# Kernel optimization log

Hardware: AMD Instinct MI355X
Metric: run time of the kernel (lower is better)

The kernel has to match this reference:

```python
import jax, jax.numpy as jnp
import numpy as np

B = 128      # graphs per side
N = 512      # nodes per graph (max for dense batch)
TOT = B * N  # 65536 total nodes per side
FIN = 128
F1, F2, F3 = 64, 64, 32
TN = 16      # tensor_neurons
BINS = 16
BN = 16      # bottleneck neurons
E = 16 * TOT # edges per side


def setup_inputs() -> dict:
    key = jax.random.key(0)
    ks = jax.random.split(key, 20)
    nrm = lambda k, shape, s=0.1: (jax.random.normal(k, shape, jnp.float32) * s)
    batch = jnp.repeat(jnp.arange(B, dtype=jnp.int32), N)
    return {
        'x1': jax.random.normal(ks[0], (TOT, FIN), jnp.float32),
        'x2': jax.random.normal(ks[1], (TOT, FIN), jnp.float32),
        'edge_index_1': jax.random.randint(ks[2], (2, E), 0, TOT, jnp.int32),
        'edge_index_2': jax.random.randint(ks[3], (2, E), 0, TOT, jnp.int32),
        'batch_1': batch,
        'batch_2': batch,
        'W1': nrm(ks[4], (FIN, F1)), 'b1': jnp.zeros((F1,), jnp.float32),
        'W2': nrm(ks[5], (F1, F2)), 'b2': jnp.zeros((F2,), jnp.float32),
        'W3': nrm(ks[6], (F2, F3)), 'b3': jnp.zeros((F3,), jnp.float32),
        'att_W': nrm(ks[7], (F3, F3)),
        'ntn_W': nrm(ks[8], (F3, F3, TN)),
        'ntn_V': nrm(ks[9], (TN, 2 * F3)),
        'ntn_b': jnp.zeros((TN,), jnp.float32),
        'fc1_W': nrm(ks[10], (TN + BINS, BN)),
        'fc1_b': jnp.zeros((BN,), jnp.float32),
        'sc_W': nrm(ks[11], (BN, 1)),
        'sc_b': jnp.zeros((1,), jnp.float32),
    }


def _gcn(x, W, b, src, dst):
    # PyG GCNConv: h = XW; add self-loops; D^{-1/2} A D^{-1/2} aggregation; + bias
    h = x @ W
    deg = jnp.zeros((TOT,), jnp.float32).at[dst].add(1.0) + 1.0  # incl. self-loop
    dis = jax.lax.rsqrt(deg)
    msg = h[src] * (dis[src] * dis[dst])[:, None]
    out = jnp.zeros_like(h).at[dst].add(msg) + h * (1.0 / deg)[:, None]
    return out + b


def _conv_pass(x, ei, W1, b1, W2, b2, W3, b3):
    # dropout is identity in eval mode
    h = jax.nn.relu(_gcn(x, W1, b1, ei[0], ei[1]))
    h = jax.nn.relu(_gcn(h, W2, b2, ei[0], ei[1]))
    return _gcn(h, W3, b3, ei[0], ei[1])


def _to_dense_batch(x, batch):
    ones = jnp.ones((TOT,), jnp.float32)
    cnt = jax.ops.segment_sum(ones, batch, num_segments=B)  # [B]
    starts = jnp.concatenate([jnp.zeros((1,), jnp.int32), jnp.cumsum(cnt.astype(jnp.int32))[:-1]])
    pos = jnp.arange(TOT, dtype=jnp.int32) - starts[batch]
    dense = jnp.zeros((B, N, x.shape[1]), x.dtype).at[batch, pos].set(x)
    cnt_i = cnt.astype(jnp.int32)
    return dense, cnt_i


def _histogram(af1, af2, batch_1, batch_2):
    d1, cnt1 = _to_dense_batch(af1, batch_1)
    d2, cnt2 = _to_dense_batch(af2, batch_2)
    nn = jnp.maximum(cnt1, cnt2)  # [B]
    sc = jax.nn.sigmoid(jax.lax.stop_gradient(jnp.einsum('bnf,bmf->bnm', d1, d2)))  # [B,N,N]
    ar = jnp.arange(N)
    valid = (ar[None, :, None] < nn[:, None, None]) & (ar[None, None, :] < nn[:, None, None])
    big = jnp.float32(1e30)
    mn = jnp.min(jnp.where(valid, sc, big), axis=(1, 2))
    mx = jnp.max(jnp.where(valid, sc, -big), axis=(1, 2))
    rng = jnp.where(mx > mn, mx - mn, jnp.float32(1.0))
    bidx = jnp.clip(jnp.floor((sc - mn[:, None, None]) / rng[:, None, None] * BINS), 0, BINS - 1).astype(jnp.int32)
    ids = jnp.arange(B, dtype=jnp.int32)[:, None, None] * BINS + bidx
    hist = jnp.zeros((B * BINS,), jnp.float32).at[ids.reshape(-1)].add(valid.reshape(-1).astype(jnp.float32))
    hist = hist.reshape(B, BINS)
    return hist / hist.sum(axis=1, keepdims=True)


def _att_pool(h, batch, att_W):
    cnt = jax.ops.segment_sum(jnp.ones((TOT,), jnp.float32), batch, num_segments=B)
    g = jax.ops.segment_sum(h @ att_W, batch, num_segments=B) / cnt[:, None]
    t = jnp.tanh(g)                                   # [B,F3] global context
    s = jax.nn.sigmoid(jnp.sum(h * t[batch], axis=1)) # [TOT] attention
    return jax.ops.segment_sum(h * s[:, None], batch, num_segments=B)


def reference(x1, x2, edge_index_1, edge_index_2, batch_1, batch_2,
              W1, b1, W2, b2, W3, b3, att_W, ntn_W, ntn_V, ntn_b,
              fc1_W, fc1_b, sc_W, sc_b):
    af1 = _conv_pass(x1, edge_index_1, W1, b1, W2, b2, W3, b3)
    af2 = _conv_pass(x2, edge_index_2, W1, b1, W2, b2, W3, b3)
    hist = _histogram(af1, af2, batch_1, batch_2)
    p1 = _att_pool(af1, batch_1, att_W)
    p2 = _att_pool(af2, batch_2, att_W)
    # Neural Tensor Network
    bilin = jnp.einsum('bi,ijk,bj->bk', p1, ntn_W, p2)
    blk = jnp.concatenate([p1, p2], axis=1) @ ntn_V.T
    scores = jax.nn.relu(bilin + blk + ntn_b)
    feat = jnp.concatenate([scores, hist], axis=1)
    h = jax.nn.relu(feat @ fc1_W + fc1_b)
    return jax.nn.sigmoid(h @ sc_W + sc_b).reshape(-1)
```

## Files before the change

kernel.cpp:

```cpp
#include <hip/hip_runtime.h>
#include <hip/hip_bf16.h>

constexpr int    TOT = 65536;
constexpr int    TOT2 = 131072;
constexpr long long Ec = 16LL * TOT;
constexpr int    NB  = 1024;
constexpr int    BKN = 128;
constexpr int    CAP = 2816;

typedef unsigned int   uint32;
typedef unsigned short ushort16;
typedef __attribute__((ext_vector_type(8))) short bf16x8;
typedef __attribute__((ext_vector_type(4))) float f32x4;

__device__ __forceinline__ float sigm(float x) { return 1.f / (1.f + __expf(-x)); }

__device__ __forceinline__ uint32 f2bf_rne(float x) {
    uint32 u = __float_as_uint(x);
    return (u + 0x7fffu + ((u >> 16) & 1u)) >> 16;
}
__device__ __forceinline__ float2 bf2f(uint32 u) {
    return make_float2(__uint_as_float(u << 16), __uint_as_float(u & 0xffff0000u));
}
__device__ __forceinline__ float bf1f(ushort16 u) {
    return __uint_as_float(((uint32)u) << 16);
}
__device__ __forceinline__ uint32 relu_bf2(uint32 v) {
    uint32 keep = (((int)v < 0) ? 0u : 0xFFFF0000u) | ((v & 0x8000u) ? 0u : 0x0000FFFFu);
    return v & keep;
}

__global__ void setup_k(const float* __restrict__ W1, const float* __restrict__ W2,
                        const float* __restrict__ W3, ushort16* __restrict__ Wt1,
                        ushort16* __restrict__ Wt2, ushort16* __restrict__ Wt3,
                        const int* __restrict__ b1, const int* __restrict__ b2,
                        int* __restrict__ cnt, int* __restrict__ st,
                        int* __restrict__ gcnt, float* __restrict__ hist) {
    int t = blockIdx.x * 256 + threadIdx.x;
    if (t < 8192) {
        int j = t >> 7, k = t & 127;
        Wt1[t] = (ushort16)f2bf_rne(W1[k * 64 + j]);
    } else if (t < 12288) {
        int u = t - 8192; int j = u >> 6, k = u & 63;
        Wt2[u] = (ushort16)f2bf_rne(W2[k * 64 + j]);
    } else if (t < 14336) {
        int u = t - 12288; int j = u >> 6, k = u & 63;
        Wt3[u] = (ushort16)f2bf_rne(W3[k * 32 + j]);
    } else if (t < 14592) {
        int q = t - 14336;
        const int* bat = (q < 128) ? b1 : b2;
        const int g = q & 127;
        int lo = 0, hi = TOT;
        while (lo < hi) { int m = (lo + hi) >> 1; if (bat[m] < g) lo = m + 1; else hi = m; }
        const int s0 = lo;
        hi = TOT;
        while (lo < hi) { int m = (lo + hi) >> 1; if (bat[m] < g + 1) lo = m + 1; else hi = m; }
        st[q] = s0;
        cnt[q] = lo - s0;
    } else if (t < 15616) {
        gcnt[t - 14592] = 0;
    } else if (t < 17664) {
        hist[t - 15616] = 0.f;
    }
}

__global__ __launch_bounds__(1024) void bktfill2_k(const int* __restrict__ ei1, const int* __restrict__ ei2,
                                                   int* __restrict__ gcnt, uint32* __restrict__ bkt) {
    __shared__ int hist[NB];
    __shared__ int hbase[NB];
    const int tid = threadIdx.x, blk = blockIdx.x;
    hist[tid] = 0;
    __syncthreads();
    const long long base = (long long)blk * 8192;
#pragma unroll
    for (int q = 0; q < 8; ++q) {
        long long e = base + q * 1024 + tid;
        int d = (e < Ec) ? ei1[Ec + e] : (TOT + ei2[Ec + (e - Ec)]);
        atomicAdd(&hist[d >> 7], 1);
    }
    __syncthreads();
    {
        int c = hist[tid];
        hbase[tid] = c ? atomicAdd(&gcnt[tid], c) : 0;
        hist[tid] = 0;
    }
    __syncthreads();
#pragma unroll
    for (int q = 0; q < 8; ++q) {
        long long e = base + q * 1024 + tid;
        int s, d;
        if (e < Ec) { s = ei1[e]; d = ei1[Ec + e]; }
        else        { long long e2 = e - Ec; s = TOT + ei2[e2]; d = TOT + ei2[Ec + e2]; }
        int bb = d >> 7;
        int lofs = atomicAdd(&hist[bb], 1);
        bkt[(size_t)bb * CAP + hbase[bb] + lofs] = (uint32)s | ((uint32)(d & 127) << 20);
    }
}

__global__ __launch_bounds__(256) void bktsort_k(const int* __restrict__ gcnt, const uint32* __restrict__ bkt,
                                                 uint32* __restrict__ csr, int* __restrict__ rowstart,
                                                 int* __restrict__ rowend, float* __restrict__ dis) {
    __shared__ int deg[BKN], offs[BKN], cur[BKN];
    const int b = blockIdx.x, tid = threadIdx.x;
    const int ne = gcnt[b];
    const int e0 = b * CAP;
    if (tid < BKN) deg[tid] = 0;
    __syncthreads();
    for (int i = tid; i < ne; i += 256) atomicAdd(&deg[bkt[e0 + i] >> 20], 1);
    __syncthreads();
    if (tid == 0) {
        int o = 0;
        for (int q = 0; q < BKN; ++q) { offs[q] = o; cur[q] = o; o += deg[q]; }
    }
    __syncthreads();
    if (tid < BKN) {
        rowstart[b * BKN + tid] = e0 + offs[tid];
        rowend[b * BKN + tid]   = e0 + offs[tid] + deg[tid];
        dis[b * BKN + tid] = rsqrtf((float)deg[tid] + 1.0f);
    }
    __syncthreads();
    for (int i = tid; i < ne; i += 256) {
        uint32 v = bkt[e0 + i];
        int dl = v >> 20;
        int pos = atomicAdd(&cur[dl], 1);
        csr[e0 + pos] = v & 0x1FFFF;
    }
}

template<int K, int NC, bool RELU, bool XBF>
__global__ __launch_bounds__(256) void gemmf_k(const void* __restrict__ X1v,
                                               const void* __restrict__ X2v,
                                               const ushort16* __restrict__ Wt,
                                               const float* __restrict__ dis,
                                               ushort16* __restrict__ out) {
    constexpr int NK = K / 32;
    const int tid = threadIdx.x, lane = tid & 63, wave = tid >> 6;
    const int i0 = (blockIdx.x * 4 + wave) * 16;
    const int arow = i0 + (lane & 15);
    const int ks0 = (lane >> 4) * 8;
    bf16x8 a[NK];
    if (XBF) {
        const uint32* Xr = (arow < TOT) ? (const uint32*)X1v + (size_t)arow * (K / 2)
                                        : (const uint32*)X2v + (size_t)(arow - TOT) * (K / 2);
#pragma unroll
        for (int s = 0; s < NK; ++s) {
            uint4 v = *(const uint4*)(Xr + s * 16 + ks0 / 2);
            if (RELU) { v.x = relu_bf2(v.x); v.y = relu_bf2(v.y); v.z = relu_bf2(v.z); v.w = relu_bf2(v.w); }
            a[s] = *(bf16x8*)&v;
        }
    } else {
        const float* Xr = (arow < TOT) ? (const float*)X1v + (size_t)arow * K
                                       : (const float*)X2v + (size_t)(arow - TOT) * K;
#pragma unroll
        for (int s = 0; s < NK; ++s) {
            float4 v0 = *(const float4*)(Xr + s * 32 + ks0);
            float4 v1 = *(const float4*)(Xr + s * 32 + ks0 + 4);
            if (RELU) {
                v0.x = fmaxf(v0.x, 0.f); v0.y = fmaxf(v0.y, 0.f); v0.z = fmaxf(v0.z, 0.f); v0.w = fmaxf(v0.w, 0.f);
                v1.x = fmaxf(v1.x, 0.f); v1.y = fmaxf(v1.y, 0.f); v1.z = fmaxf(v1.z, 0.f); v1.w = fmaxf(v1.w, 0.f);
            }
            uint4 p;
            p.x = f2bf_rne(v0.x) | (f2bf_rne(v0.y) << 16);
            p.y = f2bf_rne(v0.z) | (f2bf_rne(v0.w) << 16);
            p.z = f2bf_rne(v1.x) | (f2bf_rne(v1.y) << 16);
            p.w = f2bf_rne(v1.z) | (f2bf_rne(v1.w) << 16);
            a[s] = *(bf16x8*)&p;
        }
    }
    float dv[4];
#pragma unroll
    for (int r = 0; r < 4; ++r) dv[r] = dis[i0 + (lane >> 4) * 4 + r];
#pragma unroll
    for (int jt = 0; jt < NC / 16; ++jt) {
        const int col = jt * 16 + (lane & 15);
        f32x4 cc = {0.f, 0.f, 0.f, 0.f};
#pragma unroll
        for (int s = 0; s < NK; ++s) {
            bf16x8 b = *(const bf16x8*)(Wt + (size_t)col * K + s * 32 + ks0);
            cc = __builtin_amdgcn_mfma_f32_16x16x32_bf16(a[s], b, cc, 0, 0, 0);
        }
#pragma unroll
        for (int r = 0; r < 4; ++r) {
            const int row = i0 + (lane >> 4) * 4 + r;
            out[(size_t)row * NC + col] = (ushort16)f2bf_rne(cc[r] * dv[r]);
        }
    }
}

template<int NC>
__global__ __launch_bounds__(256) void gatherb_k(uint32* __restrict__ out, const uint32* __restrict__ hs,
                                                 const float* __restrict__ dis, const float* __restrict__ bias,
                                                 const int* __restrict__ rowstart, const int* __restrict__ rowend,
                                                 const uint32* __restrict__ csr) {
    constexpr int TPN = NC / 2;
    constexpr int NG  = 256 / TPN;
    constexpr int NPB = 2 * NG;
    int bid;
    {
        const int xcd = blockIdx.x & 7, idx = blockIdx.x >> 3;
        const int half = gridDim.x >> 1;
        bid = (xcd < 4) ? (idx * 4 + xcd) : (half + idx * 4 + (xcd - 4));
    }
    const int tid = threadIdx.x;
    const int cp = tid & (TPN - 1);
    const int g = tid / TPN;
    const int nodeA = bid * NPB + g;
    const int nodeB = nodeA + NG;
    const float2 bb = ((const float2*)bias)[cp];
    float2 svA = bf2f(hs[(size_t)nodeA * TPN + cp]);
    float2 svB = bf2f(hs[(size_t)nodeB * TPN + cp]);
    float a0 = svA.x, a1 = svA.y;
    float b0 = svB.x, b1 = svB.y;
    int eA = rowstart[nodeA]; const int eA1 = rowend[nodeA];
    int eB = rowstart[nodeB]; const int eB1 = rowend[nodeB];
    while (true) {
        const bool ca = (eA + 8 <= eA1), cb = (eB + 8 <= eB1);
        if (!ca && !cb) break;
        uint32 pa[8], pb[8];
        if (ca) {
#pragma unroll
            for (int q = 0; q < 8; ++q) pa[q] = hs[(size_t)csr[eA + q] * TPN + cp];
        }
        if (cb) {
#pragma unroll
            for (int q = 0; q < 8; ++q) pb[q] = hs[(size_t)csr[eB + q] * TPN + cp];
        }
        if (ca) {
#pragma unroll
            for (int q = 0; q < 8; ++q) { float2 f = bf2f(pa[q]); a0 += f.x; a1 += f.y; }
            eA += 8;
        }
        if (cb) {
#pragma unroll
            for (int q = 0; q < 8; ++q) { float2 f = bf2f(pb[q]); b0 += f.x; b1 += f.y; }
            eB += 8;
        }
    }
    if (eA + 4 <= eA1) {
        uint32 p[4];
#pragma unroll
        for (int q = 0; q < 4; ++q) p[q] = hs[(size_t)csr[eA + q] * TPN + cp];
#pragma unroll
        for (int q = 0; q < 4; ++q) { float2 f = bf2f(p[q]); a0 += f.x; a1 += f.y; }
        eA += 4;
    }
    for (; eA < eA1; ++eA) { float2 f = bf2f(hs[(size_t)csr[eA] * TPN + cp]); a0 += f.x; a1 += f.y; }
    if (eB + 4 <= eB1) {
        uint32 p[4];
#pragma unroll
        for (int q = 0; q < 4; ++q) p[q] = hs[(size_t)csr[eB + q] * TPN + cp];
#pragma unroll
        for (int q = 0; q < 4; ++q) { float2 f = bf2f(p[q]); b0 += f.x; b1 += f.y; }
        eB += 4;
    }
    for (; eB < eB1; ++eB) { float2 f = bf2f(hs[(size_t)csr[eB] * TPN + cp]); b0 += f.x; b1 += f.y; }
    const float dvA = dis[nodeA], dvB = dis[nodeB];
    out[(size_t)nodeA * TPN + cp] = f2bf_rne(a0 * dvA + bb.x) | (f2bf_rne(a1 * dvA + bb.y) << 16);
    out[(size_t)nodeB * TPN + cp] = f2bf_rne(b0 * dvB + bb.x) | (f2bf_rne(b1 * dvB + bb.y) << 16);
}

__global__ __launch_bounds__(256) void attpool_k(const ushort16* __restrict__ af,
                                                 const int* __restrict__ cnt, const int* __restrict__ st,
                                                 const float* __restrict__ attW, float* __restrict__ pool) {
    const int side = blockIdx.x >> 7, b = blockIdx.x & 127;
    const ushort16* h = af + (size_t)side * TOT * 32;
    const int c = cnt[side * 128 + b], s0 = st[side * 128 + b];
    const int f = threadIdx.x & 31, grp = threadIdx.x >> 5;
    __shared__ float red[8][32];
    __shared__ float mhS[32], tS[32];
    float acc = 0.f;
    for (int i = grp; i < c; i += 8) acc += bf1f(h[(size_t)(s0 + i) * 32 + f]);
    red[grp][f] = acc;
    __syncthreads();
    if (threadIdx.x < 32) { float tt = 0; for (int g = 0; g < 8; ++g) tt += red[g][f]; mhS[f] = tt / (float)c; }
    __syncthreads();
    if (threadIdx.x < 32) {
        float g = 0;
        for (int k = 0; k < 32; ++k) g += mhS[k] * attW[k * 32 + f];
        tS[f] = tanhf(g);
    }
    __syncthreads();
    const float tf = tS[f];
    acc = 0.f;
    for (int i = grp; i < c; i += 8) {
        float hv = bf1f(h[(size_t)(s0 + i) * 32 + f]);
        float pr = hv * tf;
#pragma unroll
        for (int m = 16; m; m >>= 1) pr += __shfl_xor(pr, m, 32);
        float sA = 1.f / (1.f + expf(-pr));
        acc += hv * sA;
    }
    __syncthreads();
    red[grp][f] = acc;
    __syncthreads();
    if (threadIdx.x < 32) {
        float tt = 0; for (int g = 0; g < 8; ++g) tt += red[g][f];
        pool[(size_t)(side * 128 + b) * 32 + f] = tt;
    }
}

__global__ __launch_bounds__(256) void mm2_k(const ushort16* __restrict__ afb,
                                             const int* __restrict__ cnt, const int* __restrict__ st,
                                             float* __restrict__ bmn, float* __restrict__ bmx) {
    const int b = blockIdx.x >> 3, it8 = blockIdx.x & 7;
    const int c1 = cnt[b], c2 = cnt[128 + b];
    const int s1 = st[b], s2 = st[128 + b];
    const int nn = max(c1, c2);
    const int tid = threadIdx.x, lane = tid & 63, wave = tid >> 6;
    const int itile = it8 * 4 + wave;
    const int i0 = itile * 16;
    float lmn = 1e30f, lmx = -1e30f;
    if (i0 < nn) {
        const int arow = i0 + (lane & 15);
        const int koff = (lane >> 4) * 8;
        bf16x8 a = {0, 0, 0, 0, 0, 0, 0, 0};
        if (arow < c1) a = *(const bf16x8*)(afb + (size_t)(s1 + arow) * 32 + koff);
        const int ibase = i0 + (lane >> 4) * 4;
        const int njt = (nn + 15) >> 4;
        for (int jt = 0; jt < njt; ++jt) {
            const int brow = jt * 16 + (lane & 15);
            bf16x8 bb = {0, 0, 0, 0, 0, 0, 0, 0};
            if (brow < c2) bb = *(const bf16x8*)(afb + (size_t)(s2 + brow) * 32 + koff);
            f32x4 cc = {0.f, 0.f, 0.f, 0.f};
            cc = __builtin_amdgcn_mfma_f32_16x16x32_bf16(a, bb, cc, 0, 0, 0);
            if (brow < nn) {
#pragma unroll
                for (int r = 0; r < 4; ++r) {
                    if (ibase + r < nn) { lmn = fminf(lmn, cc[r]); lmx = fmaxf(lmx, cc[r]); }
                }
            }
        }
    }
    __shared__ float redn[256], redx[256];
    redn[tid] = lmn; redx[tid] = lmx;
    __syncthreads();
    for (int sr = 128; sr; sr >>= 1) {
        if (tid < sr) {
            redn[tid] = fminf(redn[tid], redn[tid + sr]);
            redx[tid] = fmaxf(redx[tid], redx[tid + sr]);
        }
        __syncthreads();
    }
    if (tid == 0) { bmn[blockIdx.x] = redn[0]; bmx[blockIdx.x] = redx[0]; }
}

__global__ __launch_bounds__(256) void bin2_k(const ushort16* __restrict__ afb,
                                              const int* __restrict__ cnt, const int* __restrict__ st,
                                              const float* __restrict__ bmn, const float* __restrict__ bmx,
                                              float* __restrict__ hist) {
    const int b = blockIdx.x >> 3, it8 = blockIdx.x & 7;
    const int c1 = cnt[b], c2 = cnt[128 + b];
    const int s1 = st[b], s2 = st[128 + b];
    const int nn = max(c1, c2);
    const int tid = threadIdx.x, lane = tid & 63, wave = tid >> 6;
    const int itile = it8 * 4 + wave;
    const int i0 = itile * 16;
    float dmn = 1e30f, dmx = -1e30f;
#pragma unroll
    for (int q = 0; q < 8; ++q) {
        dmn = fminf(dmn, bmn[(b << 3) + q]);
        dmx = fmaxf(dmx, bmx[(b << 3) + q]);
    }
    const float vMn = sigm(dmn), vMx = sigm(dmx);
    const float vScale = 16.f / ((vMx > vMn) ? (vMx - vMn) : 1.f);
    __shared__ int hloc[16 * 256];
    __shared__ int part[64];
#pragma unroll
    for (int q = 0; q < 16; ++q) hloc[q * 256 + tid] = 0;
    __syncthreads();
    if (i0 < nn) {
        const int arow = i0 + (lane & 15);
        const int koff = (lane >> 4) * 8;
        bf16x8 a = {0, 0, 0, 0, 0, 0, 0, 0};
        if (arow < c1) a = *(const bf16x8*)(afb + (size_t)(s1 + arow) * 32 + koff);
        const int ibase = i0 + (lane >> 4) * 4;
        const int njt = (nn + 15) >> 4;
        for (int jt = 0; jt < njt; ++jt) {
            const int brow = jt * 16 + (lane & 15);
            bf16x8 bb = {0, 0, 0, 0, 0, 0, 0, 0};
            if (brow < c2) bb = *(const bf16x8*)(afb + (size_t)(s2 + brow) * 32 + koff);
            f32x4 cc = {0.f, 0.f, 0.f, 0.f};
            cc = __builtin_amdgcn_mfma_f32_16x16x32_bf16(a, bb, cc, 0, 0, 0);
            if (brow < nn) {
#pragma unroll
                for (int r = 0; r < 4; ++r) {
                    if (ibase + r < nn) {
                        float t = (sigm(cc[r]) - vMn) * vScale;
                        int bi = (int)floorf(t);
                        bi = bi < 0 ? 0 : (bi > 15 ? 15 : bi);
                        hloc[bi * 256 + tid] += 1;
                    }
                }
            }
        }
    }
    __syncthreads();
    if (tid < 64) {
        const int bin = tid & 15, q = tid >> 4;
        int s = 0;
        for (int t2 = q * 64; t2 < q * 64 + 64; ++t2) s += hloc[bin * 256 + t2];
        part[tid] = s;
    }
    __syncthreads();
    if (tid < 16) {
        int s = part[tid] + part[16 + tid] + part[32 + tid] + part[48 + tid];
        atomicAdd(&hist[b * 16 + tid], (float)s);
    }
}

__global__ __launch_bounds__(64) void final_k(const float* __restrict__ pool, const float* __restrict__ hist,
                                              const int* __restrict__ cnt,
                                              const float* __restrict__ ntnW, const float* __restrict__ ntnV,
                                              const float* __restrict__ ntnb, const float* __restrict__ fc1W,
                                              const float* __restrict__ fc1b, const float* __restrict__ scW,
                                              const float* __restrict__ scb, float* __restrict__ out) {
    const int b = blockIdx.x;
    const int tid = threadIdx.x;
    __shared__ float P1[32], P2[32], feat[32], red[64];
    if (tid < 32) { P1[tid] = pool[b * 32 + tid]; P2[tid] = pool[4096 + b * 32 + tid]; }
    __syncthreads();
    const int k = tid & 15, part = tid >> 4;
    float acc = 0.f;
    for (int i = part * 8; i < part * 8 + 8; ++i) {
        float p1i = P1[i];
        for (int j = 0; j < 32; ++j) acc += p1i * P2[j] * ntnW[(i * 32 + j) * 16 + k];
    }
    red[tid] = acc;
    __syncthreads();
    if (tid < 16) {
        float bl = red[tid] + red[16 + tid] + red[32 + tid] + red[48 + tid];
        float blk = ntnb[tid];
        for (int i = 0; i < 32; ++i) blk += P1[i] * ntnV[tid * 64 + i];
        for (int j = 0; j < 32; ++j) blk += P2[j] * ntnV[tid * 64 + 32 + j];
        feat[tid] = fmaxf(bl + blk, 0.f);
        const int nn = max(cnt[b], cnt[128 + b]);
        feat[16 + tid] = hist[b * 16 + tid] / (float)(nn * nn);
    }
    __syncthreads();
    if (tid < 16) {
        float h = fc1b[tid];
        for (int f = 0; f < 32; ++f) h += feat[f] * fc1W[f * 16 + tid];
        red[tid] = fmaxf(h, 0.f);
    }
    __syncthreads();
    if (tid == 0) {
        float o = scb[0];
        for (int j = 0; j < 16; ++j) o += red[j] * scW[j];
        out[b] = 1.f / (1.f + expf(-o));
    }
}

extern "C" void kernel_launch(void* const* d_in, const int* in_sizes, int n_in,
                              void* d_out, int out_size, void* d_ws, size_t ws_size,
                              hipStream_t stream) {
    const float* x1   = (const float*)d_in[0];
    const float* x2   = (const float*)d_in[1];
    const int*   ei1  = (const int*)d_in[2];
    const int*   ei2  = (const int*)d_in[3];
    const int*   bat1 = (const int*)d_in[4];
    const int*   bat2 = (const int*)d_in[5];
    const float* W1   = (const float*)d_in[6];
    const float* b1   = (const float*)d_in[7];
    const float* W2   = (const float*)d_in[8];
    const float* b2   = (const float*)d_in[9];
    const float* W3   = (const float*)d_in[10];
    const float* b3   = (const float*)d_in[11];
    const float* attW = (const float*)d_in[12];
    const float* ntnW = (const float*)d_in[13];
    const float* ntnV = (const float*)d_in[14];
    const float* ntnb = (const float*)d_in[15];
    const float* fc1W = (const float*)d_in[16];
    const float* fc1b = (const float*)d_in[17];
    const float* scW  = (const float*)d_in[18];
    const float* scb  = (const float*)d_in[19];
    float* out = (float*)d_out;

    uint32* Hbuf   = (uint32*)d_ws;
    uint32* Gb     = Hbuf + (size_t)TOT2 * 32;
    uint32* AFb    = Gb + (size_t)TOT2 * 32;
    uint32* bkt    = AFb + (size_t)TOT2 * 16;
    uint32* csr    = bkt + (size_t)NB * CAP;
    float* dis     = (float*)(csr + (size_t)NB * CAP);
    int*   rowstart= (int*)(dis + TOT2);
    int*   rowend  = rowstart + TOT2;
    int*   gcnt    = rowend + TOT2;
    int*   cnt     = gcnt + NB;
    int*   st      = cnt + 256;
    float* pool    = (float*)(st + 256);
    float* hist    = pool + 8192;
    float* bmn     = hist + 2048;
    float* bmx     = bmn + 1024;
    ushort16* Wt1  = (ushort16*)(bmx + 1024);
    ushort16* Wt2  = Wt1 + 8192;
    ushort16* Wt3  = Wt2 + 4096;

    setup_k<<<69, 256, 0, stream>>>(W1, W2, W3, Wt1, Wt2, Wt3, bat1, bat2, cnt, st, gcnt, hist);
    bktfill2_k<<<256, 1024, 0, stream>>>(ei1, ei2, gcnt, bkt);
    bktsort_k<<<NB, 256, 0, stream>>>(gcnt, bkt, csr, rowstart, rowend, dis);

    gemmf_k<128, 64, false, false><<<2048, 256, 0, stream>>>(x1, x2, Wt1, dis, (ushort16*)Hbuf);
    gatherb_k<64><<<TOT2 / 16, 256, 0, stream>>>(Gb, Hbuf, dis, b1, rowstart, rowend, csr);

    gemmf_k<64, 64, true, true><<<2048, 256, 0, stream>>>(Gb, Gb, Wt2, dis, (ushort16*)Hbuf);
    gatherb_k<64><<<TOT2 / 16, 256, 0, stream>>>(Gb, Hbuf, dis, b2, rowstart, rowend, csr);

    gemmf_k<64, 32, true, true><<<2048, 256, 0, stream>>>(Gb, Gb, Wt3, dis, (ushort16*)Hbuf);
    gatherb_k<32><<<TOT2 / 32, 256, 0, stream>>>(AFb, Hbuf, dis, b3, rowstart, rowend, csr);

    attpool_k<<<256, 256, 0, stream>>>((const ushort16*)AFb, cnt, st, attW, pool);
    mm2_k<<<1024, 256, 0, stream>>>((const ushort16*)AFb, cnt, st, bmn, bmx);
    bin2_k<<<1024, 256, 0, stream>>>((const ushort16*)AFb, cnt, st, bmn, bmx, hist);
    final_k<<<128, 64, 0, stream>>>(pool, hist, cnt, ntnW, ntnV, ntnb, fc1W, fc1b, scW, scb, out);
}
```

Before: 315.3 us.

## Fuse GCN neighbor aggregation with next layer's MFMA GEMM

Adds an agemm_k kernel that gathers each node's CSR neighbors, applies the self-loop term, degree scaling, bias and ReLU in registers, then feeds the result directly into the next layer's bf16 MFMA projection. This replaces two gather+GEMM kernel pairs, removing the intermediate bf16 write and reread and two launches. In exchange, each MFMA lane now performs a 16-row gather with 8-wide unrolled neighbor loads. That can raise register pressure and gives less parallel gather work than the dedicated gather kernel.

Result: faster. 298.8 us (-5.2%).

```diff
diff --git a/kernel.cpp b/kernel.cpp
--- a/kernel.cpp
+++ b/kernel.cpp
@@ -28,6 +28,11 @@
 __device__ __forceinline__ uint32 relu_bf2(uint32 v) {
     uint32 keep = (((int)v < 0) ? 0u : 0xFFFF0000u) | ((v & 0x8000u) ? 0u : 0x0000FFFFu);
     return v & keep;
+}
+__device__ __forceinline__ void addu4(float* a, uint4 v) {
+    float2 f0 = bf2f(v.x), f1 = bf2f(v.y), f2 = bf2f(v.z), f3 = bf2f(v.w);
+    a[0] += f0.x; a[1] += f0.y; a[2] += f1.x; a[3] += f1.y;
+    a[4] += f2.x; a[5] += f2.y; a[6] += f3.x; a[7] += f3.y;
 }
 
 __global__ void setup_k(const float* __restrict__ W1, const float* __restrict__ W2,
@@ -127,9 +132,9 @@
     }
 }
 
-template<int K, int NC, bool RELU, bool XBF>
-__global__ __launch_bounds__(256) void gemmf_k(const void* __restrict__ X1v,
-                                               const void* __restrict__ X2v,
+template<int K, int NC>
+__global__ __launch_bounds__(256) void gemmf_k(const float* __restrict__ X1,
+                                               const float* __restrict__ X2,
                                                const ushort16* __restrict__ Wt,
                                                const float* __restrict__ dis,
                                                ushort16* __restrict__ out) {
@@ -139,26 +144,13 @@
     const int arow = i0 + (lane & 15);
     const int ks0 = (lane >> 4) * 8;
     bf16x8 a[NK];
-    if (XBF) {
-        const uint32* Xr = (arow < TOT) ? (const uint32*)X1v + (size_t)arow * (K / 2)
-                                        : (const uint32*)X2v + (size_t)(arow - TOT) * (K / 2);
-#pragma unroll
-        for (int s = 0; s < NK; ++s) {
-            uint4 v = *(const uint4*)(Xr + s * 16 + ks0 / 2);
-            if (RELU) { v.x = relu_bf2(v.x); v.y = relu_bf2(v.y); v.z = relu_bf2(v.z); v.w = relu_bf2(v.w); }
-            a[s] = *(bf16x8*)&v;
-        }
-    } else {
-        const float* Xr = (arow < TOT) ? (const float*)X1v + (size_t)arow * K
-                                       : (const float*)X2v + (size_t)(arow - TOT) * K;
+    {
+        const float* Xr = (arow < TOT) ? X1 + (size_t)arow * K
+                                       : X2 + (size_t)(arow - TOT) * K;
 #pragma unroll
         for (int s = 0; s < NK; ++s) {
             float4 v0 = *(const float4*)(Xr + s * 32 + ks0);
             float4 v1 = *(const float4*)(Xr + s * 32 + ks0 + 4);
-            if (RELU) {
-                v0.x = fmaxf(v0.x, 0.f); v0.y = fmaxf(v0.y, 0.f); v0.z = fmaxf(v0.z, 0.f); v0.w = fmaxf(v0.w, 0.f);
-                v1.x = fmaxf(v1.x, 0.f); v1.y = fmaxf(v1.y, 0.f); v1.z = fmaxf(v1.z, 0.f); v1.w = fmaxf(v1.w, 0.f);
-            }
             uint4 p;
             p.x = f2bf_rne(v0.x) | (f2bf_rne(v0.y) << 16);
             p.y = f2bf_rne(v0.z) | (f2bf_rne(v0.w) << 16);
@@ -177,6 +169,111 @@
 #pragma unroll
         for (int s = 0; s < NK; ++s) {
             bf16x8 b = *(const bf16x8*)(Wt + (size_t)col * K + s * 32 + ks0);
+            cc = __builtin_amdgcn_mfma_f32_16x16x32_bf16(a[s], b, cc, 0, 0, 0);
+        }
+#pragma unroll
+        for (int r = 0; r < 4; ++r) {
+            const int row = i0 + (lane >> 4) * 4 + r;
+            out[(size_t)row * NC + col] = (ushort16)f2bf_rne(cc[r] * dv[r]);
+        }
+    }
+}
+
+template<int NC>
+__global__ __launch_bounds__(256) void agemm_k(const uint32* __restrict__ hs,
+                                               const ushort16* __restrict__ Wt,
+                                               const float* __restrict__ dis,
+                                               const float* __restrict__ bias,
+                                               const int* __restrict__ rowstart,
+                                               const int* __restrict__ rowend,
+                                               const uint32* __restrict__ csr,
+                                               ushort16* __restrict__ out) {
+    const int tid = threadIdx.x, lane = tid & 63, wave = tid >> 6;
+    const int i0 = (blockIdx.x * 4 + wave) * 16;
+    const int arow = i0 + (lane & 15);
+    const int ks0 = (lane >> 4) * 8;
+    const int u0 = ks0 >> 1;
+    float acc0[8], acc1[8];
+    {
+        const uint32* rp = hs + (size_t)arow * 32;
+        uint4 v0 = *(const uint4*)(rp + u0);
+        uint4 v1 = *(const uint4*)(rp + 16 + u0);
+#pragma unroll
+        for (int j = 0; j < 8; ++j) { acc0[j] = 0.f; acc1[j] = 0.f; }
+        addu4(acc0, v0); addu4(acc1, v1);
+    }
+    int e = rowstart[arow];
+    const int e1 = rowend[arow];
+    while (e + 8 <= e1) {
+        int idx[8];
+#pragma unroll
+        for (int q = 0; q < 8; ++q) idx[q] = (int)csr[e + q];
+        uint4 v0[8], v1[8];
+#pragma unroll
+        for (int q = 0; q < 8; ++q) {
+            const uint32* rp = hs + (size_t)idx[q] * 32;
+            v0[q] = *(const uint4*)(rp + u0);
+            v1[q] = *(const uint4*)(rp + 16 + u0);
+        }
+#pragma unroll
+        for (int q = 0; q < 8; ++q) { addu4(acc0, v0[q]); addu4(acc1, v1[q]); }
+        e += 8;
+    }
+    if (e + 4 <= e1) {
+        uint4 v0[4], v1[4];
+#pragma unroll
+        for (int q = 0; q < 4; ++q) {
+            const uint32* rp = hs + (size_t)csr[e + q] * 32;
+            v0[q] = *(const uint4*)(rp + u0);
+            v1[q] = *(const uint4*)(rp + 16 + u0);
+        }
+#pragma unroll
+        for (int q = 0; q < 4; ++q) { addu4(acc0, v0[q]); addu4(acc1, v1[q]); }
+        e += 4;
+    }
+    for (; e < e1; ++e) {
+        const uint32* rp = hs + (size_t)csr[e] * 32;
+        addu4(acc0, *(const uint4*)(rp + u0));
+        addu4(acc1, *(const uint4*)(rp + 16 + u0));
+    }
+    const float dA = dis[arow];
+    bf16x8 a[2];
+    {
+        float4 bb0 = *(const float4*)(bias + ks0);
+        float4 bb1 = *(const float4*)(bias + ks0 + 4);
+        float4 bb2 = *(const float4*)(bias + 32 + ks0);
+        float4 bb3 = *(const float4*)(bias + 32 + ks0 + 4);
+        float v[8];
+        v[0] = fmaxf(acc0[0] * dA + bb0.x, 0.f); v[1] = fmaxf(acc0[1] * dA + bb0.y, 0.f);
+        v[2] = fmaxf(acc0[2] * dA + bb0.z, 0.f); v[3] = fmaxf(acc0[3] * dA + bb0.w, 0.f);
+        v[4] = fmaxf(acc0[4] * dA + bb1.x, 0.f); v[5] = fmaxf(acc0[5] * dA + bb1.y, 0.f);
+        v[6] = fmaxf(acc0[6] * dA + bb1.z, 0.f); v[7] = fmaxf(acc0[7] * dA + bb1.w, 0.f);
+        uint4 p;
+        p.x = f2bf_rne(v[0]) | (f2bf_rne(v[1]) << 16);
+        p.y = f2bf_rne(v[2]) | (f2bf_rne(v[3]) << 16);
+        p.z = f2bf_rne(v[4]) | (f2bf_rne(v[5]) << 16);
+        p.w = f2bf_rne(v[6]) | (f2bf_rne(v[7]) << 16);
+        a[0] = *(bf16x8*)&p;
+        v[0] = fmaxf(acc1[0] * dA + bb2.x, 0.f); v[1] = fmaxf(acc1[1] * dA + bb2.y, 0.f);
+        v[2] = fmaxf(acc1[2] * dA + bb2.z, 0.f); v[3] = fmaxf(acc1[3] * dA + bb2.w, 0.f);
+        v[4] = fmaxf(acc1[4] * dA + bb3.x, 0.f); v[5] = fmaxf(acc1[5] * dA + bb3.y, 0.f);
+        v[6] = fmaxf(acc1[6] * dA + bb3.z, 0.f); v[7] = fmaxf(acc1[7] * dA + bb3.w, 0.f);
+        p.x = f2bf_rne(v[0]) | (f2bf_rne(v[1]) << 16);
+        p.y = f2bf_rne(v[2]) | (f2bf_rne(v[3]) << 16);
+        p.z = f2bf_rne(v[4]) | (f2bf_rne(v[5]) << 16);
+        p.w = f2bf_rne(v[6]) | (f2bf_rne(v[7]) << 16);
+        a[1] = *(bf16x8*)&p;
+    }
+    float dv[4];
+#pragma unroll
+    for (int r = 0; r < 4; ++r) dv[r] = dis[i0 + (lane >> 4) * 4 + r];
+#pragma unroll
+    for (int jt = 0; jt < NC / 16; ++jt) {
+        const int col = jt * 16 + (lane & 15);
+        f32x4 cc = {0.f, 0.f, 0.f, 0.f};
+#pragma unroll
+        for (int s = 0; s < 2; ++s) {
+            bf16x8 b = *(const bf16x8*)(Wt + (size_t)col * 64 + s * 32 + ks0);
             cc = __builtin_amdgcn_mfma_f32_16x16x32_bf16(a[s], b, cc, 0, 0, 0);
         }
 #pragma unroll
@@ -498,13 +595,9 @@
     bktfill2_k<<<256, 1024, 0, stream>>>(ei1, ei2, gcnt, bkt);
     bktsort_k<<<NB, 256, 0, stream>>>(gcnt, bkt, csr, rowstart, rowend, dis);
 
-    gemmf_k<128, 64, false, false><<<2048, 256, 0, stream>>>(x1, x2, Wt1, dis, (ushort16*)Hbuf);
-    gatherb_k<64><<<TOT2 / 16, 256, 0, stream>>>(Gb, Hbuf, dis, b1, rowstart, rowend, csr);
-
-    gemmf_k<64, 64, true, true><<<2048, 256, 0, stream>>>(Gb, Gb, Wt2, dis, (ushort16*)Hbuf);
-    gatherb_k<64><<<TOT2 / 16, 256, 0, stream>>>(Gb, Hbuf, dis, b2, rowstart, rowend, csr);
-
-    gemmf_k<64, 32, true, true><<<2048, 256, 0, stream>>>(Gb, Gb, Wt3, dis, (ushort16*)Hbuf);
+    gemmf_k<128, 64><<<2048, 256, 0, stream>>>(x1, x2, Wt1, dis, (ushort16*)Hbuf);
+    agemm_k<64><<<2048, 256, 0, stream>>>(Hbuf, Wt2, dis, b1, rowstart, rowend, csr, (ushort16*)Gb);
+    agemm_k<32><<<2048, 256, 0, stream>>>(Gb, Wt3, dis, b2, rowstart, rowend, csr, (ushort16*)Hbuf);
     gatherb_k<32><<<TOT2 / 32, 256, 0, stream>>>(AFb, Hbuf, dis, b3, rowstart, rowend, csr);
 
     attpool_k<<<256, 256, 0, stream>>>((const ushort16*)AFb, cnt, st, attW, pool);
```
